# Kernel tuning notes

Measured on AMD Instinct MI355X. Metric: run time of the kernel, lower is better.

The kernel has to match this reference:

```python
import jax, jax.numpy as jnp
import numpy as np

H, W, F, V, D = 1024, 1024, 100000, 50000, 32


def setup_inputs() -> dict:
    key = jax.random.key(0)
    k1, k2, k3, k4 = jax.random.split(key, 4)
    pix_to_face = jax.random.randint(k1, (H, W), 0, F, dtype=jnp.int64 if jax.config.read('jax_enable_x64') else jnp.int32)
    bg = jax.random.uniform(k2, (H, W)) < 0.1
    pix_to_face = jnp.where(bg, -1, pix_to_face)
    bary = jax.random.uniform(k2, (H, W, 3), dtype=jnp.float32)
    bary_coords = bary / jnp.sum(bary, axis=-1, keepdims=True)  # barycentric: sums to 1
    faces = jax.random.randint(k3, (F, 3), 0, V, dtype=pix_to_face.dtype)
    attributes = jax.random.normal(k4, (V, D), dtype=jnp.float32)
    return {"pix_to_face": pix_to_face, "bary_coords": bary_coords,
            "faces": faces, "attributes": attributes}


def reference(pix_to_face, bary_coords, faces, attributes):
    # faces[pix_to_face]: (H, W, 3) vertex indices (torch -1 wraps to last face)
    vertices_idx = jnp.take(faces, pix_to_face, axis=0, mode='wrap')
    # attributes[vertices_idx]: (H, W, 3, D)
    vertex_attribute = jnp.take(attributes, vertices_idx, axis=0, mode='wrap')
    # barycentric weighted sum over the 3 face vertices -> (H, W, D)
    attribute_map = jnp.einsum('hwk,hwkd->hwd', bary_coords, vertex_attribute)
    mask = pix_to_face != -1
    return attribute_map, mask
```

## Files before the change

### kernel.cpp

```cpp
#include <hip/hip_runtime.h>
#include <hip/hip_bf16.h>


typedef float fvec4 __attribute__((ext_vector_type(4)));

__global__ __launch_bounds__(256) void Renderer_interp_kernel(
    const int* __restrict__ pix,
    const float* __restrict__ bary,
    const int* __restrict__ faces,
    const float* __restrict__ attr,
    float* __restrict__ out,
    float* __restrict__ mask,
    int npix, int F)
{
    int tid = blockIdx.x * blockDim.x + threadIdx.x;
    int p = tid >> 3;
    int t = tid & 7;
    if (p >= npix) return;

    int fraw = pix[p];
    int f = (fraw < 0) ? (fraw + F) : fraw;

    int base = 3 * f;
    int v0 = faces[base + 0];
    int v1 = faces[base + 1];
    int v2 = faces[base + 2];

    float w0 = bary[3 * p + 0];
    float w1 = bary[3 * p + 1];
    float w2 = bary[3 * p + 2];

    const fvec4* A = reinterpret_cast<const fvec4*>(attr);
    const fvec4* a0 = A + ((size_t)v0 * 8 + t);
    const fvec4* a1 = A + ((size_t)v1 * 8 + t);
    const fvec4* a2 = A + ((size_t)v2 * 8 + t);

    fvec4 r0, r1, r2;
    asm volatile(
        "global_load_dwordx4 %0, %3, off sc0\n\t"
        "global_load_dwordx4 %1, %4, off sc0\n\t"
        "global_load_dwordx4 %2, %5, off sc0\n\t"
        "s_waitcnt vmcnt(0)"
        : "=&v"(r0), "=&v"(r1), "=&v"(r2)
        : "v"(a0), "v"(a1), "v"(a2)
        : "memory");

    fvec4 o = w0 * r0 + w1 * r1 + w2 * r2;

    reinterpret_cast<fvec4*>(out)[(size_t)p * 8 + t] = o;

    if (t == 0) {
        mask[p] = (fraw != -1) ? 1.0f : 0.0f;
    }
}

extern "C" void kernel_launch(void* const* d_in, const int* in_sizes, int n_in,
                              void* d_out, int out_size, void* d_ws, size_t ws_size,
                              hipStream_t stream) {
    const int*   pix   = (const int*)d_in[0];
    const float* bary  = (const float*)d_in[1];
    const int*   faces = (const int*)d_in[2];
    const float* attr  = (const float*)d_in[3];

    int npix = in_sizes[0];
    int F    = in_sizes[2] / 3;

    float* out  = (float*)d_out;
    float* mask = (float*)d_out + (size_t)npix * 32;

    int total = npix * 8;
    int block = 256;
    int grid = (total + block - 1) / block;
    Renderer_interp_kernel<<<grid, block, 0, stream>>>(pix, bary, faces, attr,
                                                       out, mask, npix, F);
}
```

Measured before the change: 65.54 us.

## Precompute per-face bf16 attribute table and gather contiguously per pixel

A new pre-pass kernel gathers the three vertex attribute rows of every face, converts them to bf16 and writes them into a contiguous 256-byte record per face in workspace. The per-pixel kernel then reads one face record instead of reading the faces array and gathering three separate fp32 vertex rows, cutting the dependent index load and the gathered bytes per pixel. In exchange it adds a second launch, a table build over all faces that reads and writes tens of MB, and bf16 rounding of the attributes, which loosens accuracy. The original path is kept as a fallback when the workspace is too small.

```diff
diff --git a/kernel.cpp b/kernel.cpp
--- a/kernel.cpp
+++ b/kernel.cpp
@@ -3,12 +3,57 @@
 
 
 typedef float fvec4 __attribute__((ext_vector_type(4)));
+typedef unsigned short usvec8 __attribute__((ext_vector_type(8)));
+typedef unsigned short usvec4 __attribute__((ext_vector_type(4)));
 
-__global__ __launch_bounds__(256) void Renderer_interp_kernel(
+__device__ __forceinline__ float bf16_to_f32(unsigned short h) {
+    unsigned int u = ((unsigned int)h) << 16;
+    return __builtin_bit_cast(float, u);
+}
+
+__device__ __forceinline__ unsigned short f32_to_bf16(float x) {
+    unsigned int u = __builtin_bit_cast(unsigned int, x);
+    unsigned int r = (u + 0x7FFFu + ((u >> 16) & 1u)) >> 16;
+    return (unsigned short)r;
+}
+
+__global__ __launch_bounds__(256) void Renderer_facetab_kernel(
+    const int* __restrict__ faces,
+    const float* __restrict__ attr,
+    unsigned short* __restrict__ table,
+    int F)
+{
+    int tid = blockIdx.x * blockDim.x + threadIdx.x;
+    if (tid >= F * 8) return;
+    int f = tid >> 3;
+    int t = tid & 7;
+
+    int v0 = faces[3 * f + 0];
+    int v1 = faces[3 * f + 1];
+    int v2 = faces[3 * f + 2];
+
+    const fvec4* A = reinterpret_cast<const fvec4*>(attr);
+    fvec4 c0 = A[v0 * 8 + t];
+    fvec4 c1 = A[v1 * 8 + t];
+    fvec4 c2 = A[v2 * 8 + t];
+
+    usvec8 rec;
+    rec[0] = f32_to_bf16(c0[0]); rec[1] = f32_to_bf16(c0[1]);
+    rec[2] = f32_to_bf16(c0[2]); rec[3] = f32_to_bf16(c0[3]);
+    rec[4] = f32_to_bf16(c1[0]); rec[5] = f32_to_bf16(c1[1]);
+    rec[6] = f32_to_bf16(c1[2]); rec[7] = f32_to_bf16(c1[3]);
+    reinterpret_cast<usvec8*>(table)[f * 16 + t] = rec;
+
+    usvec4 r2;
+    r2[0] = f32_to_bf16(c2[0]); r2[1] = f32_to_bf16(c2[1]);
+    r2[2] = f32_to_bf16(c2[2]); r2[3] = f32_to_bf16(c2[3]);
+    *reinterpret_cast<usvec4*>(table + (size_t)f * 128 + 64 + t * 4) = r2;
+}
+
+__global__ __launch_bounds__(256) void Renderer_interp_face_kernel(
     const int* __restrict__ pix,
     const float* __restrict__ bary,
-    const int* __restrict__ faces,
-    const float* __restrict__ attr,
+    const unsigned short* __restrict__ table,
     float* __restrict__ out,
     float* __restrict__ mask,
     int npix, int F)
@@ -21,37 +66,48 @@
     int fraw = pix[p];
     int f = (fraw < 0) ? (fraw + F) : fraw;
 
-    int base = 3 * f;
-    int v0 = faces[base + 0];
-    int v1 = faces[base + 1];
-    int v2 = faces[base + 2];
-
     float w0 = bary[3 * p + 0];
     float w1 = bary[3 * p + 1];
     float w2 = bary[3 * p + 2];
 
-    const fvec4* A = reinterpret_cast<const fvec4*>(attr);
-    const fvec4* a0 = A + ((size_t)v0 * 8 + t);
-    const fvec4* a1 = A + ((size_t)v1 * 8 + t);
-    const fvec4* a2 = A + ((size_t)v2 * 8 + t);
+    usvec8 r01 = reinterpret_cast<const usvec8*>(table)[f * 16 + t];
+    usvec4 r2 = *reinterpret_cast<const usvec4*>(
+        table + (size_t)f * 128 + 64 + t * 4);
 
-    fvec4 r0, r1, r2;
-    asm volatile(
-        "global_load_dwordx4 %0, %3, off sc0\n\t"
-        "global_load_dwordx4 %1, %4, off sc0\n\t"
-        "global_load_dwordx4 %2, %5, off sc0\n\t"
-        "s_waitcnt vmcnt(0)"
-        : "=&v"(r0), "=&v"(r1), "=&v"(r2)
-        : "v"(a0), "v"(a1), "v"(a2)
-        : "memory");
-
-    fvec4 o = w0 * r0 + w1 * r1 + w2 * r2;
+    fvec4 o;
+    #pragma unroll
+    for (int j = 0; j < 4; ++j) {
+        o[j] = w0 * bf16_to_f32(r01[j])
+             + w1 * bf16_to_f32(r01[j + 4])
+             + w2 * bf16_to_f32(r2[j]);
+    }
 
     reinterpret_cast<fvec4*>(out)[(size_t)p * 8 + t] = o;
 
     if (t == 0) {
         mask[p] = (fraw != -1) ? 1.0f : 0.0f;
     }
+}
+
+__global__ __launch_bounds__(256) void Renderer_interp_kernel(
+    const int* __restrict__ pix, const float* __restrict__ bary,
+    const int* __restrict__ faces, const float* __restrict__ attr,
+    float* __restrict__ out, float* __restrict__ mask, int npix, int F)
+{
+    int tid = blockIdx.x * blockDim.x + threadIdx.x;
+    int p = tid >> 3;
+    int t = tid & 7;
+    if (p >= npix) return;
+    int fraw = pix[p];
+    int f = (fraw < 0) ? (fraw + F) : fraw;
+    int base = 3 * f;
+    int v0 = faces[base + 0], v1 = faces[base + 1], v2 = faces[base + 2];
+    float w0 = bary[3 * p + 0], w1 = bary[3 * p + 1], w2 = bary[3 * p + 2];
+    const fvec4* A = reinterpret_cast<const fvec4*>(attr);
+    fvec4 r0 = A[v0 * 8 + t], r1 = A[v1 * 8 + t], r2 = A[v2 * 8 + t];
+    fvec4 o = w0 * r0 + w1 * r1 + w2 * r2;
+    reinterpret_cast<fvec4*>(out)[(size_t)p * 8 + t] = o;
+    if (t == 0) mask[p] = (fraw != -1) ? 1.0f : 0.0f;
 }
 
 extern "C" void kernel_launch(void* const* d_in, const int* in_sizes, int n_in,
@@ -68,9 +124,19 @@
     float* out  = (float*)d_out;
     float* mask = (float*)d_out + (size_t)npix * 32;
 
-    int total = npix * 8;
-    int block = 256;
-    int grid = (total + block - 1) / block;
-    Renderer_interp_kernel<<<grid, block, 0, stream>>>(pix, bary, faces, attr,
-                                                       out, mask, npix, F);
+    size_t need = (size_t)F * 256;
+
+    if (ws_size >= need) {
+        unsigned short* table = (unsigned short*)d_ws;
+        int nprep = F * 8;
+        Renderer_facetab_kernel<<<(nprep + 255) / 256, 256, 0, stream>>>(
+            faces, attr, table, F);
+        int total = npix * 8;
+        Renderer_interp_face_kernel<<<(total + 255) / 256, 256, 0, stream>>>(
+            pix, bary, table, out, mask, npix, F);
+    } else {
+        int total = npix * 8;
+        Renderer_interp_kernel<<<(total + 255) / 256, 256, 0, stream>>>(
+            pix, bary, faces, attr, out, mask, npix, F);
+    }
 }
```

Result: slower. 68.66 us (+4.8%).
